# Performance work log

Measured on AMD Instinct MI355X. Metric: run time of the kernel, lower is better.

The kernel has to match this reference:

```python
import jax, jax.numpy as jnp
import numpy as np

E = 8  # path_num


def setup_inputs() -> dict:
    key = jax.random.key(0)
    k1, k2, k3 = jax.random.split(key, 3)
    N, D = 8192, 1024
    x = jax.random.normal(k1, (N, D), dtype=jnp.float32)
    hot_mask = jax.random.randint(k2, (N, E), 0, 2, dtype=jnp.int32)  # multi-hot 0/1
    score = jax.random.uniform(k3, (N, E), dtype=jnp.float32)
    return {"x": x, "hot_mask": hot_mask, "score": score}


def reference(x, hot_mask, score):
    # MoE dispatch (route_logic='1d', transform=True):
    # for each expert e, gather tokens n with hot_mask[n, e] == 1 in order,
    # scaled by score[n, e]. Outputs padded to capacity N (zeros beyond count).
    N, D = x.shape
    mask = hot_mask > 0                                   # [N, E]
    ranks = jnp.cumsum(hot_mask, axis=0) - 1              # [N, E] position within expert
    dest = jnp.where(mask, ranks, N)                      # dropped tokens -> dump slot N
    tags = jnp.arange(N, dtype=jnp.int64)                 # flow_tag (arange via pack_invalid_flow)
    scale = score * mask.astype(score.dtype)              # [N, E]

    def per_expert(dest_e, scale_e, mask_e):
        vals = x * scale_e[:, None]                       # [N, D] scaled (zero if not routed)
        out = jnp.zeros((N + 1, D), x.dtype).at[dest_e].add(vals)[:N]
        tag_out = jnp.zeros((N + 1,), jnp.int64).at[dest_e].add(
            jnp.where(mask_e, tags, 0))[:N]               # gathered out_flow_tag, 0-padded
        return out, tag_out

    out_data, out_tags = jax.vmap(per_expert, in_axes=(1, 1, 1))(dest, scale, mask)
    counts = jnp.sum(hot_mask, axis=0)                    # [E] tokens per expert
    return out_data, out_tags, counts
```

## Files before the change

kernel.cpp:

```cpp
#include <hip/hip_runtime.h>

#define N_TOK 8192
#define D_DIM 1024
#define E_NUM 8
#define D4 (D_DIM / 4)


__global__ __launch_bounds__(256) void dispatch_scan_kernel(
    const int* __restrict__ hot_mask,
    int* __restrict__ dest,
    int* __restrict__ counts_i,
    float* __restrict__ out_tags,
    float* __restrict__ out_counts)
{
    const int e = blockIdx.x;
    const int t = threadIdx.x;
    constexpr int TPT = N_TOK / 256;

    __shared__ int lds[256];

    const int base = t * TPT;
    int m[TPT];
    int tot = 0;
    #pragma unroll
    for (int i = 0; i < TPT; ++i) {
        m[i] = hot_mask[(size_t)(base + i) * E_NUM + e];
        tot += m[i];
    }

    lds[t] = tot;
    __syncthreads();

    for (int off = 1; off < 256; off <<= 1) {
        int other = (t >= off) ? lds[t - off] : 0;
        __syncthreads();
        if (t >= off) lds[t] += other;
        __syncthreads();
    }

    const int incl  = lds[t];
    const int excl  = incl - tot;
    const int count = lds[255];

    int r = excl;
    #pragma unroll
    for (int i = 0; i < TPT; ++i) {
        const int n = base + i;
        if (m[i]) {
            dest[(size_t)n * E_NUM + e]     = r;
            out_tags[(size_t)e * N_TOK + r] = (float)n;
            ++r;
        } else {
            dest[(size_t)n * E_NUM + e] = -1;
        }
    }

    for (int rr = count + t; rr < N_TOK; rr += 256) {
        out_tags[(size_t)e * N_TOK + rr] = 0.0f;
    }

    if (t == 0) {
        counts_i[e]   = count;
        out_counts[e] = (float)count;
    }
}

__global__ __launch_bounds__(256) void dispatch_scatter_kernel(
    const float4* __restrict__ x,
    const float* __restrict__ score,
    const int* __restrict__ dest,
    const int* __restrict__ counts_i,
    float4* __restrict__ out)
{
    const int b = blockIdx.x;
    const int c = threadIdx.x;

    if (b < N_TOK) {
        const int n = b;
        const float4 xv = x[(size_t)n * D4 + c];
        #pragma unroll
        for (int e = 0; e < E_NUM; ++e) {
            const int r = dest[(size_t)n * E_NUM + e];
            if (r >= 0) {
                const float s = score[(size_t)n * E_NUM + e];
                float4 v;
                v.x = xv.x * s;
                v.y = xv.y * s;
                v.z = xv.z * s;
                v.w = xv.w * s;
                out[((size_t)e * N_TOK + r) * D4 + c] = v;
            }
        }
    } else {
        const int row = b - N_TOK;
        const int e   = row >> 13;
        const int r   = row & (N_TOK - 1);
        if (r >= counts_i[e]) {
            float4 z;
            z.x = 0.0f; z.y = 0.0f; z.z = 0.0f; z.w = 0.0f;
            out[(size_t)row * D4 + c] = z;
        }
    }
}

extern "C" void kernel_launch(void* const* d_in, const int* in_sizes, int n_in,
                              void* d_out, int out_size, void* d_ws, size_t ws_size,
                              hipStream_t stream) {
    const float* x        = (const float*)d_in[0];
    const int*   hot_mask = (const int*)d_in[1];
    const float* score    = (const float*)d_in[2];

    float* out        = (float*)d_out;
    float* out_data   = out;
    float* out_tags   = out + (size_t)E_NUM * N_TOK * D_DIM;
    float* out_counts = out_tags + (size_t)E_NUM * N_TOK;

    int* dest     = (int*)d_ws;
    int* counts_i = dest + (size_t)N_TOK * E_NUM;

    dispatch_scan_kernel<<<E_NUM, 256, 0, stream>>>(
        hot_mask, dest, counts_i, out_tags, out_counts);

    dispatch_scatter_kernel<<<N_TOK + E_NUM * N_TOK, 256, 0, stream>>>(
        (const float4*)x, score, dest, counts_i, (float4*)out_data);
}
```

Measured before the change: 63.03 us.

## Parallelize routing scan with packed 16-bit lanes across 32 blocks

Replaces the 8-block per-expert serial scan with a 32-block scan that packs all eight expert counts into two 64-bit words as 16-bit lanes, so one prefix sum covers every expert at once. The scatter kernel adds up the preceding block totals itself and takes over writing the tags and counts. This is meant to cut the latency of the small, poorly parallel scan kernel that runs before the bandwidth-bound scatter. The cost is redundant summing of block totals in every scatter block. Correctness also relies on each per-block count fitting in 16 bits, which holds for 256 tokens per block.

```diff
diff --git a/kernel.cpp b/kernel.cpp
--- a/kernel.cpp
+++ b/kernel.cpp
@@ -4,101 +4,120 @@
 #define D_DIM 1024
 #define E_NUM 8
 #define D4 (D_DIM / 4)
+#define SCAN_BLOCKS 32
+
+typedef unsigned long long u64;
 
 
-__global__ __launch_bounds__(256) void dispatch_scan_kernel(
-    const int* __restrict__ hot_mask,
-    int* __restrict__ dest,
-    int* __restrict__ counts_i,
-    float* __restrict__ out_tags,
-    float* __restrict__ out_counts)
+__global__ __launch_bounds__(256) void scan_kernel(
+    const int4* __restrict__ mask4,
+    ulonglong2* __restrict__ prefix,
+    ulonglong2* __restrict__ bsum)
 {
-    const int e = blockIdx.x;
-    const int t = threadIdx.x;
-    constexpr int TPT = N_TOK / 256;
+    const int t   = threadIdx.x;
+    const int n   = blockIdx.x * 256 + t;
 
-    __shared__ int lds[256];
+    const int4 a = mask4[(size_t)n * 2];
+    const int4 b = mask4[(size_t)n * 2 + 1];
 
-    const int base = t * TPT;
-    int m[TPT];
-    int tot = 0;
-    #pragma unroll
-    for (int i = 0; i < TPT; ++i) {
-        m[i] = hot_mask[(size_t)(base + i) * E_NUM + e];
-        tot += m[i];
-    }
+    u64 lo = (u64)a.x | ((u64)a.y << 16) | ((u64)a.z << 32) | ((u64)a.w << 48);
+    u64 hi = (u64)b.x | ((u64)b.y << 16) | ((u64)b.z << 32) | ((u64)b.w << 48);
 
-    lds[t] = tot;
+    __shared__ u64 slo[256], shi[256];
+    slo[t] = lo; shi[t] = hi;
     __syncthreads();
 
     for (int off = 1; off < 256; off <<= 1) {
-        int other = (t >= off) ? lds[t - off] : 0;
+        u64 plo = 0, phi = 0;
+        if (t >= off) { plo = slo[t - off]; phi = shi[t - off]; }
         __syncthreads();
-        if (t >= off) lds[t] += other;
+        if (t >= off) { slo[t] += plo; shi[t] += phi; }
         __syncthreads();
     }
 
-    const int incl  = lds[t];
-    const int excl  = incl - tot;
-    const int count = lds[255];
+    ulonglong2 ex;
+    ex.x = slo[t] - lo;
+    ex.y = shi[t] - hi;
+    prefix[n] = ex;
 
-    int r = excl;
-    #pragma unroll
-    for (int i = 0; i < TPT; ++i) {
-        const int n = base + i;
-        if (m[i]) {
-            dest[(size_t)n * E_NUM + e]     = r;
-            out_tags[(size_t)e * N_TOK + r] = (float)n;
-            ++r;
-        } else {
-            dest[(size_t)n * E_NUM + e] = -1;
-        }
-    }
-
-    for (int rr = count + t; rr < N_TOK; rr += 256) {
-        out_tags[(size_t)e * N_TOK + rr] = 0.0f;
-    }
-
-    if (t == 0) {
-        counts_i[e]   = count;
-        out_counts[e] = (float)count;
+    if (t == 255) {
+        ulonglong2 tot; tot.x = slo[255]; tot.y = shi[255];
+        bsum[blockIdx.x] = tot;
     }
 }
 
-__global__ __launch_bounds__(256) void dispatch_scatter_kernel(
+__global__ __launch_bounds__(256) void scatter_kernel(
     const float4* __restrict__ x,
     const float* __restrict__ score,
-    const int* __restrict__ dest,
-    const int* __restrict__ counts_i,
-    float4* __restrict__ out)
+    const int4* __restrict__ mask4,
+    const ulonglong2* __restrict__ prefix,
+    const ulonglong2* __restrict__ bsum,
+    float4* __restrict__ out_data,
+    float* __restrict__ out_tags,
+    float* __restrict__ out_counts)
 {
     const int b = blockIdx.x;
     const int c = threadIdx.x;
 
     if (b < N_TOK) {
-        const int n = b;
+        const int n   = b;
+        const int bid = n >> 8;
+
+        u64 plo = prefix[n].x, phi = prefix[n].y;
+        for (int k = 0; k < bid; ++k) {
+            ulonglong2 s = bsum[k];
+            plo += s.x; phi += s.y;
+        }
+
+        const int4 ma = mask4[(size_t)n * 2];
+        const int4 mb = mask4[(size_t)n * 2 + 1];
+        const float4* sc4 = (const float4*)(score + (size_t)n * E_NUM);
+        const float4 s0 = sc4[0];
+        const float4 s1 = sc4[1];
+
         const float4 xv = x[(size_t)n * D4 + c];
+
+        const int me[8] = { ma.x, ma.y, ma.z, ma.w, mb.x, mb.y, mb.z, mb.w };
+        const float se[8] = { s0.x, s0.y, s0.z, s0.w, s1.x, s1.y, s1.z, s1.w };
+
         #pragma unroll
         for (int e = 0; e < E_NUM; ++e) {
-            const int r = dest[(size_t)n * E_NUM + e];
-            if (r >= 0) {
-                const float s = score[(size_t)n * E_NUM + e];
+            if (me[e]) {
+                const u64 p = (e < 4) ? plo : phi;
+                const int r = (int)((p >> (16 * (e & 3))) & 0xFFFF);
+                const float s = se[e];
                 float4 v;
-                v.x = xv.x * s;
-                v.y = xv.y * s;
-                v.z = xv.z * s;
-                v.w = xv.w * s;
-                out[((size_t)e * N_TOK + r) * D4 + c] = v;
+                v.x = xv.x * s; v.y = xv.y * s; v.z = xv.z * s; v.w = xv.w * s;
+                out_data[((size_t)e * N_TOK + r) * D4 + c] = v;
+                if (c == 0) out_tags[(size_t)e * N_TOK + r] = (float)n;
             }
         }
     } else {
         const int row = b - N_TOK;
         const int e   = row >> 13;
         const int r   = row & (N_TOK - 1);
-        if (r >= counts_i[e]) {
-            float4 z;
-            z.x = 0.0f; z.y = 0.0f; z.z = 0.0f; z.w = 0.0f;
-            out[(size_t)row * D4 + c] = z;
+
+        if (row == 0 && c < E_NUM) {
+            const int sh = 16 * (c & 3);
+            int cnt = 0;
+            for (int k = 0; k < SCAN_BLOCKS; ++k) {
+                const u64 p = (c < 4) ? bsum[k].x : bsum[k].y;
+                cnt += (int)((p >> sh) & 0xFFFF);
+            }
+            out_counts[c] = (float)cnt;
+        }
+
+        const int sh = 16 * (e & 3);
+        int cnt = 0;
+        for (int k = 0; k < SCAN_BLOCKS; ++k) {
+            const u64 p = (e < 4) ? bsum[k].x : bsum[k].y;
+            cnt += (int)((p >> sh) & 0xFFFF);
+        }
+
+        if (r >= cnt) {
+            float4 z; z.x = 0.0f; z.y = 0.0f; z.z = 0.0f; z.w = 0.0f;
+            out_data[(size_t)row * D4 + c] = z;
+            if (c == 0) out_tags[row] = 0.0f;
         }
     }
 }
@@ -115,12 +134,13 @@
     float* out_tags   = out + (size_t)E_NUM * N_TOK * D_DIM;
     float* out_counts = out_tags + (size_t)E_NUM * N_TOK;
 
-    int* dest     = (int*)d_ws;
-    int* counts_i = dest + (size_t)N_TOK * E_NUM;
+    ulonglong2* prefix = (ulonglong2*)d_ws;
+    ulonglong2* bsum   = prefix + N_TOK;
 
-    dispatch_scan_kernel<<<E_NUM, 256, 0, stream>>>(
-        hot_mask, dest, counts_i, out_tags, out_counts);
+    scan_kernel<<<SCAN_BLOCKS, 256, 0, stream>>>(
+        (const int4*)hot_mask, prefix, bsum);
 
-    dispatch_scatter_kernel<<<N_TOK + E_NUM * N_TOK, 256, 0, stream>>>(
-        (const float4*)x, score, dest, counts_i, (float4*)out_data);
+    scatter_kernel<<<N_TOK + E_NUM * N_TOK, 256, 0, stream>>>(
+        (const float4*)x, score, (const int4*)hot_mask, prefix, bsum,
+        (float4*)out_data, out_tags, out_counts);
 }
```

New measurement: 102.6 us. +62.7%, slower.
